# Kernel tuning notes

Hardware: AMD Instinct MI355X
Metric: run time of the kernel (lower is better)

Reference implementation:

```python
import jax, jax.numpy as jnp
import numpy as np

C = 256
C8 = C // 8
B, D, H, W = 1, 8, 32, 32
N = D * H * W


def setup_inputs() -> dict:
    key = jax.random.key(0)
    ks = jax.random.split(key, 16)
    s = 0.02
    inp = {
        'x': jax.random.normal(ks[0], (B, C, D, H, W), dtype=jnp.float32),
        'WqA': jax.random.normal(ks[1], (C8, C), dtype=jnp.float32) * s,
        'bqA': jnp.zeros((C8,), dtype=jnp.float32),
        'WkA': jax.random.normal(ks[2], (C8, C), dtype=jnp.float32) * s,
        'bkA': jnp.zeros((C8,), dtype=jnp.float32),
        'WvA': jax.random.normal(ks[3], (C, C), dtype=jnp.float32) * s,
        'bvA': jnp.zeros((C,), dtype=jnp.float32),
        'WqB': jax.random.normal(ks[4], (C8, C), dtype=jnp.float32) * s,
        'bqB': jnp.zeros((C8,), dtype=jnp.float32),
        'WkB': jax.random.normal(ks[5], (C8, C), dtype=jnp.float32) * s,
        'bkB': jnp.zeros((C8,), dtype=jnp.float32),
        'WvB': jax.random.normal(ks[6], (C, C), dtype=jnp.float32) * s,
        'bvB': jnp.zeros((C,), dtype=jnp.float32),
        'gamma_A': jax.random.normal(ks[7], (1,), dtype=jnp.float32) * 0.5,
        'gamma_B': jax.random.normal(ks[8], (1,), dtype=jnp.float32) * 0.5,
    }
    return inp


def _conv1x1(Wt, b, xf):
    # 1x1x1 Conv3d on flattened volume: [Cout,Cin] x [B,Cin,N] -> [B,Cout,N]
    return jnp.einsum('oc,bcn->bon', Wt, xf) + b[None, :, None]


def reference(x, WqA, bqA, WkA, bkA, WvA, bvA, WqB, bqB, WkB, bkB, WvB, bvB, gamma_A, gamma_B):
    b_, c_, d_, h_, w_ = x.shape
    n = d_ * h_ * w_
    xf = x.reshape(b_, c_, n)  # [B,C,N]

    QA = _conv1x1(WqA, bqA, xf)  # [B,C8,N]
    KA = _conv1x1(WkA, bkA, xf)
    VA = _conv1x1(WvA, bvA, xf)  # [B,C,N]
    QB = _conv1x1(WqB, bqB, xf)
    KB = _conv1x1(WkB, bkB, xf)
    VB = _conv1x1(WvB, bvB, xf)

    # attention_B_A[b,n,m] = softmax_m( QB^T KA )
    attn_BA = jax.nn.softmax(jnp.einsum('bcn,bcm->bnm', QB, KA), axis=-1)
    # F_B_new = V_A @ attn_BA^T
    F_B = jnp.einsum('bcm,bnm->bcn', VA, attn_BA).reshape(b_, c_, d_, h_, w_)

    attn_AB = jax.nn.softmax(jnp.einsum('bcn,bcm->bnm', QA, KB), axis=-1)
    F_A = jnp.einsum('bcm,bnm->bcn', VB, attn_AB).reshape(b_, c_, d_, h_, w_)

    out_task1 = gamma_A[0] * F_A + x
    out_task2 = gamma_B[0] * F_B + x
    return (out_task1, out_task2)
```

## Files before the change

kernel.cpp:

```cpp
#include <hip/hip_runtime.h>

#define N 8192
#define CIN 256
#define C8 32
#define QBLK 64
#define KVB 64
#define L2E 1.4426950408889634f

typedef __attribute__((ext_vector_type(8))) short short8;
typedef __attribute__((ext_vector_type(4))) float f32x4;
typedef __attribute__((ext_vector_type(4))) float float4_;
typedef __attribute__((ext_vector_type(4))) unsigned short ushort4_;
typedef __attribute__((ext_vector_type(2))) unsigned uint2_;

#define OFF_QTA 0u
#define OFF_KTA 262144u
#define OFF_QTB 524288u
#define OFF_KTB 786432u
#define OFF_VA  1048576u
#define OFF_VB  3145728u
#define PROJ_USHORTS 5242880u

__device__ __forceinline__ unsigned short f2bf(float f) {
    unsigned u = __builtin_bit_cast(unsigned, f);
    u += 0x7fffu + ((u >> 16) & 1u);
    return (unsigned short)(u >> 16);
}
__device__ __forceinline__ unsigned packbf2(float a, float b) {
    return (unsigned)f2bf(a) | ((unsigned)f2bf(b) << 16);
}
__device__ __forceinline__ float bf2f(unsigned short u) {
    return __builtin_bit_cast(float, (unsigned)u << 16);
}

__global__ __launch_bounds__(256) void castw_kernel(
    const float* __restrict__ WqA, const float* __restrict__ WkA, const float* __restrict__ WvA,
    const float* __restrict__ WqB, const float* __restrict__ WkB, const float* __restrict__ WvB,
    unsigned short* __restrict__ Wb)
{
    const int idx = blockIdx.x * 256 + threadIdx.x;
    const int e = idx * 4;
    const int r = e >> 8;
    const float* src; int rel;
    if (r < 32)       { src = WqA; rel = e; }
    else if (r < 64)  { src = WkA; rel = e - 32 * 256; }
    else if (r < 320) { src = WvA; rel = e - 64 * 256; }
    else if (r < 352) { src = WqB; rel = e - 320 * 256; }
    else if (r < 384) { src = WkB; rel = e - 352 * 256; }
    else              { src = WvB; rel = e - 384 * 256; }
    const float sc = (r < 32 || (r >= 320 && r < 352)) ? L2E : 1.0f;
    float4_ v = *(const float4_*)(src + rel);
    ushort4_ o;
    o.x = f2bf(v.x * sc); o.y = f2bf(v.y * sc); o.z = f2bf(v.z * sc); o.w = f2bf(v.w * sc);
    *(ushort4_*)(Wb + e) = o;
}

__global__ __launch_bounds__(512) void proj_kernel(
    const float* __restrict__ x, const unsigned short* __restrict__ Wb,
    const float* __restrict__ bqA, const float* __restrict__ bkA, const float* __restrict__ bvA,
    const float* __restrict__ bqB, const float* __restrict__ bkB, const float* __restrict__ bvB,
    unsigned short* __restrict__ ws)
{
    __shared__ __align__(16) unsigned short xT[32 * 256];

    const int tid = threadIdx.x;
    const int w = tid >> 6, l = tid & 63, g = l >> 4, lc = l & 15;
    const int n0 = blockIdx.x * 32;

    #pragma unroll
    for (int r = 0; r < 4; ++r) {
        const int flat4 = r * 512 + tid;
        const int c = flat4 >> 3, nl = (flat4 & 7) * 4;
        float4_ v = *(const float4_*)(x + (size_t)c * N + n0 + nl);
        #pragma unroll
        for (int e = 0; e < 4; ++e) {
            const int nn = nl + e;
            const int byte = nn * 512 + ((2 * c) ^ ((nn & 7) << 4));
            *(unsigned short*)((char*)xT + byte) = f2bf(v[e]);
        }
    }
    __syncthreads();

    f32x4 acc[5][2];
    #pragma unroll
    for (int i = 0; i < 5; ++i)
        #pragma unroll
        for (int ns = 0; ns < 2; ++ns) acc[i][ns] = (f32x4){0.f, 0.f, 0.f, 0.f};

    for (int c0 = 0; c0 < 256; c0 += 32) {
        short8 xf[2];
        #pragma unroll
        for (int ns = 0; ns < 2; ++ns) {
            const int byte = (ns * 16 + lc) * 512 + ((2 * (c0 + 8 * g)) ^ ((lc & 7) << 4));
            xf[ns] = *(const short8*)((const char*)xT + byte);
        }
        #pragma unroll
        for (int i = 0; i < 5; ++i) {
            const int ot = w * 5 + i;
            const short8 wf = *(const short8*)(Wb + (size_t)(ot * 16 + lc) * 256 + c0 + 8 * g);
            const bool isV = (ot >= 4 && ot < 20) || (ot >= 24);
            #pragma unroll
            for (int ns = 0; ns < 2; ++ns)
                acc[i][ns] = isV
                    ? __builtin_amdgcn_mfma_f32_16x16x32_bf16(wf, xf[ns], acc[i][ns], 0, 0, 0)
                    : __builtin_amdgcn_mfma_f32_16x16x32_bf16(xf[ns], wf, acc[i][ns], 0, 0, 0);
        }
    }

    #pragma unroll
    for (int i = 0; i < 5; ++i) {
        const int ot = w * 5 + i;
        const float* bias; unsigned short* dst; int orelm; bool isV = false; float bsc = 1.0f;
        if (ot < 2)       { bias = bqA; dst = ws + OFF_QTA; orelm = ot * 16;        bsc = L2E; }
        else if (ot < 4)  { bias = bkA; dst = ws + OFF_KTA; orelm = (ot - 2) * 16; }
        else if (ot < 20) { bias = bvA; dst = ws + OFF_VA;  orelm = (ot - 4) * 16;  isV = true; }
        else if (ot < 22) { bias = bqB; dst = ws + OFF_QTB; orelm = (ot - 20) * 16; bsc = L2E; }
        else if (ot < 24) { bias = bkB; dst = ws + OFF_KTB; orelm = (ot - 22) * 16; }
        else              { bias = bvB; dst = ws + OFF_VB;  orelm = (ot - 24) * 16; isV = true; }

        if (isV) {
            #pragma unroll
            for (int ii = 0; ii < 4; ++ii) {
                const float b = bias[orelm + 4 * g + ii];
                #pragma unroll
                for (int ns = 0; ns < 2; ++ns)
                    dst[(size_t)(orelm + 4 * g + ii) * N + n0 + ns * 16 + lc] = f2bf(acc[i][ns][ii] + b);
            }
        } else {
            const float b = bias[orelm + lc] * bsc;
            #pragma unroll
            for (int ns = 0; ns < 2; ++ns)
                #pragma unroll
                for (int ii = 0; ii < 4; ++ii)
                    dst[(size_t)(n0 + ns * 16 + 4 * g + ii) * C8 + orelm + lc] = f2bf(acc[i][ns][ii] + b);
        }
    }
}

__global__ __launch_bounds__(512, 4) void attn_kernel(
    const unsigned short* __restrict__ ws,
    unsigned short* __restrict__ accb,
    float* __restrict__ Lpart,
    int SP)
{
    __shared__ __align__(16) unsigned short Vt[2][256 * 64];
    __shared__ __align__(16) unsigned short Pl[2][64 * 64];

    const int tid = threadIdx.x;
    const int w = tid >> 6, l = tid & 63, g = l >> 4, lc = l & 15;
    const int bid = blockIdx.x;
    const int dir = bid & 1;
    const int qb  = (bid >> 1) & 127;
    const int sp  = bid >> 8;
    const int mlen   = N / SP;
    const int m_base = sp * mlen;
    const int NS     = mlen / KVB;

    const unsigned short* qt = ws + (dir ? OFF_QTA : OFF_QTB);
    const unsigned short* kt = ws + (dir ? OFF_KTB : OFF_KTA);
    const unsigned short* V  = ws + (dir ? OFF_VB  : OFF_VA);

    const bool sw = (w < 4);
    const int col = w * 16 + lc;

    short8 qf = {};
    if (sw) qf = *(const short8*)(qt + (size_t)(qb * QBLK + col) * C8 + 8 * g);

    const int src_c   = w * 32 + (l >> 3);
    const int src_swz = ((l & 7) ^ ((l >> 3) & 7)) << 3;
    #define STAGE(vb, mo)                                                                 \
        _Pragma("unroll")                                                                 \
        for (int h = 0; h < 4; ++h) {                                                     \
            const unsigned short* srcp = V + (size_t)(src_c + 8 * h) * N + (mo) + src_swz; \
            __builtin_amdgcn_global_load_lds(                                             \
                (const __attribute__((address_space(1))) unsigned*)srcp,                  \
                (__attribute__((address_space(3))) unsigned*)(&Vt[vb][(w * 32 + h * 8) * 64]), \
                16, 0, 0);                                                                \
        }

    STAGE(0, m_base)

    short8 kf[4], kfn[4];
    if (sw) {
        #pragma unroll
        for (int t = 0; t < 4; ++t)
            kf[t] = *(const short8*)(kt + (size_t)(m_base + 16 * t + lc) * C8 + 8 * g);
    }

    f32x4 acc[2][4];
    #pragma unroll
    for (int u = 0; u < 2; ++u)
        #pragma unroll
        for (int j = 0; j < 4; ++j) acc[u][j] = (f32x4){0.f, 0.f, 0.f, 0.f};
    float Lr = 0.f;

    for (int s = 0; s < NS; ++s) {
        const int m0 = m_base + s * KVB;
        const int pb = s & 1;

        if (sw) {
            if (s + 1 < NS) {
                #pragma unroll
                for (int t = 0; t < 4; ++t)
                    kfn[t] = *(const short8*)(kt + (size_t)(m0 + KVB + 16 * t + lc) * C8 + 8 * g);
            }
            f32x4 sv[4];
            #pragma unroll
            for (int t = 0; t < 4; ++t)
                sv[t] = __builtin_amdgcn_mfma_f32_16x16x32_bf16(kf[t], qf, (f32x4){0.f,0.f,0.f,0.f}, 0, 0, 0);

            float pr[4][4];
            #pragma unroll
            for (int t = 0; t < 4; ++t)
                #pragma unroll
                for (int i = 0; i < 4; ++i) {
                    pr[t][i] = __builtin_amdgcn_exp2f(sv[t][i]);
                    Lr += pr[t][i];
                }
            #pragma unroll
            for (int t = 0; t < 4; ++t) {
                uint2_ u2;
                u2.x = packbf2(pr[t][0], pr[t][1]);
                u2.y = packbf2(pr[t][2], pr[t][3]);
                const int byte = col * 128 + ((((2 * t + (g >> 1)) ^ (col & 7)) << 4)) + ((g & 1) << 3);
                *(uint2_*)((char*)Pl[pb] + byte) = u2;
            }
        }

        __syncthreads();

        if (s + 1 < NS) STAGE(pb ^ 1, m0 + KVB)

        __builtin_amdgcn_s_setprio(1);
        short8 vf[2][2];
        #pragma unroll
        for (int u = 0; u < 2; ++u)
            #pragma unroll
            for (int kc = 0; kc < 2; ++kc)
                vf[u][kc] = *(const short8*)((const char*)Vt[pb]
                              + (w * 32 + u * 16 + lc) * 128 + (((kc * 4 + g) ^ (lc & 7)) << 4));
        #pragma unroll
        for (int kc = 0; kc < 2; ++kc) {
            short8 pf[4];
            #pragma unroll
            for (int j = 0; j < 4; ++j)
                pf[j] = *(const short8*)((const char*)Pl[pb]
                          + (j * 16 + lc) * 128 + (((kc * 4 + g) ^ (lc & 7)) << 4));
            #pragma unroll
            for (int u = 0; u < 2; ++u)
                #pragma unroll
                for (int j = 0; j < 4; ++j)
                    acc[u][j] = __builtin_amdgcn_mfma_f32_16x16x32_bf16(vf[u][kc], pf[j], acc[u][j], 0, 0, 0);
        }
        __builtin_amdgcn_s_setprio(0);

        if (sw && s + 1 < NS) {
            #pragma unroll
            for (int t = 0; t < 4; ++t) kf[t] = kfn[t];
        }
    }

    if (sw) {
        Lr += __shfl_xor(Lr, 16);
        Lr += __shfl_xor(Lr, 32);
    }
    const size_t blk = (size_t)(dir * 128 + qb) * SP + sp;
    unsigned short* ab = accb + blk * (256 * 64);
    #pragma unroll
    for (int u = 0; u < 2; ++u)
        #pragma unroll
        for (int j = 0; j < 4; ++j)
            #pragma unroll
            for (int i = 0; i < 4; ++i) {
                const int c  = w * 32 + u * 16 + 4 * g + i;
                const int nl = j * 16 + lc;
                ab[c * 64 + nl] = f2bf(acc[u][j][i]);
            }
    if (sw && l < 16) Lpart[blk * 64 + w * 16 + l] = Lr;
}

__global__ __launch_bounds__(256) void combine_kernel(
    const float* __restrict__ x,
    const unsigned short* __restrict__ accb,
    const float* __restrict__ Lpart,
    const float* __restrict__ gammaA, const float* __restrict__ gammaB,
    float* __restrict__ out, int SP)
{
    const int tid = blockIdx.x * 256 + threadIdx.x;
    const int nl0 = (tid & 7) * 8;
    const int qb  = (tid >> 3) & 127;
    const int c   = (tid >> 10) & 255;
    const int dir = (tid >> 18) & 1;

    const size_t bb = (size_t)(dir * 128 + qb) * SP;
    float s[8], Ls[8];
    #pragma unroll
    for (int e = 0; e < 8; ++e) { s[e] = 0.f; Ls[e] = 0.f; }

    for (int sp = 0; sp < SP; ++sp) {
        const unsigned short* ap = accb + (bb + sp) * (256 * 64) + (size_t)c * 64 + nl0;
        const short8 av = *(const short8*)ap;
        const float* lp = Lpart + (bb + sp) * 64 + nl0;
        #pragma unroll
        for (int e = 0; e < 8; ++e) {
            s[e]  += bf2f((unsigned short)av[e]);
            Ls[e] += lp[e];
        }
    }

    const float gamma = dir ? gammaA[0] : gammaB[0];
    const size_t off = (size_t)c * N + qb * QBLK + nl0;
    const float* xp = x + off;
    float* op = out + (dir ? 0 : (size_t)CIN * N) + off;
    #pragma unroll
    for (int e = 0; e < 8; ++e) op[e] = gamma * s[e] / Ls[e] + xp[e];
}

extern "C" void kernel_launch(void* const* d_in, const int* in_sizes, int n_in,
                              void* d_out, int out_size, void* d_ws, size_t ws_size,
                              hipStream_t stream) {
    const float* x = (const float*)d_in[0];
    unsigned short* ws = (unsigned short*)d_ws;

    size_t needed4 = (size_t)PROJ_USHORTS * 2 + 4ull * 8388608 + 4ull * 65536;
    size_t needed2 = (size_t)PROJ_USHORTS * 2 + 2ull * 8388608 + 2ull * 65536;
    int SP = (ws_size >= needed4) ? 4 : (ws_size >= needed2) ? 2 : 1;

    unsigned short* accb = ws + PROJ_USHORTS;
    unsigned short* Wb   = accb;
    float* Lpart = (float*)(ws + PROJ_USHORTS + (size_t)SP * 4194304);

    castw_kernel<<<160, 256, 0, stream>>>(
        (const float*)d_in[1], (const float*)d_in[3], (const float*)d_in[5],
        (const float*)d_in[7], (const float*)d_in[9], (const float*)d_in[11], Wb);

    proj_kernel<<<256, 512, 0, stream>>>(
        x, Wb,
        (const float*)d_in[2],  (const float*)d_in[4],  (const float*)d_in[6],
        (const float*)d_in[8],  (const float*)d_in[10], (const float*)d_in[12],
        ws);

    attn_kernel<<<256 * SP, 512, 0, stream>>>(ws, accb, Lpart, SP);

    combine_kernel<<<2048, 256, 0, stream>>>(
        x, accb, Lpart,
        (const float*)d_in[13], (const float*)d_in[14],
        (float*)d_out, SP);
}
```

Baseline: 224.9 us.

## Restructure attention kernel: 128-query tiles, V in registers, drop LDS V staging

The attention kernel now handles 128 queries per block with all 8 waves computing scores, instead of 64 queries with half the waves idle during the score phase. V fragments are loaded from global memory straight into registers and double-buffered there, replacing the LDS staging through global_load_lds. The PV product is retiled so each wave owns a 64x64 output tile. The projection and combine kernels switch to vectorized packed stores to match the new layouts, and the split-K factor drops to at most 2, which halves the grid. The change raises register pressure and cuts block count, which risks lower occupancy and load balance.

New measurement: 319.4 us. 1.42x slower.

```diff
diff --git a/kernel.cpp b/kernel.cpp
--- a/kernel.cpp
+++ b/kernel.cpp
@@ -3,7 +3,7 @@
 #define N 8192
 #define CIN 256
 #define C8 32
-#define QBLK 64
+#define QBLK 128
 #define KVB 64
 #define L2E 1.4426950408889634f
 
@@ -102,8 +102,8 @@
             #pragma unroll
             for (int ns = 0; ns < 2; ++ns)
                 acc[i][ns] = isV
-                    ? __builtin_amdgcn_mfma_f32_16x16x32_bf16(wf, xf[ns], acc[i][ns], 0, 0, 0)
-                    : __builtin_amdgcn_mfma_f32_16x16x32_bf16(xf[ns], wf, acc[i][ns], 0, 0, 0);
+                    ? __builtin_amdgcn_mfma_f32_16x16x32_bf16(xf[ns], wf, acc[i][ns], 0, 0, 0)
+                    : __builtin_amdgcn_mfma_f32_16x16x32_bf16(wf, xf[ns], acc[i][ns], 0, 0, 0);
         }
     }
 
@@ -119,164 +119,149 @@
         else              { bias = bvB; dst = ws + OFF_VB;  orelm = (ot - 24) * 16; isV = true; }
 
         if (isV) {
-            #pragma unroll
-            for (int ii = 0; ii < 4; ++ii) {
-                const float b = bias[orelm + 4 * g + ii];
-                #pragma unroll
-                for (int ns = 0; ns < 2; ++ns)
-                    dst[(size_t)(orelm + 4 * g + ii) * N + n0 + ns * 16 + lc] = f2bf(acc[i][ns][ii] + b);
+            const float b = bias[orelm + lc];
+            #pragma unroll
+            for (int ns = 0; ns < 2; ++ns) {
+                ushort4_ pk;
+                pk.x = f2bf(acc[i][ns][0] + b); pk.y = f2bf(acc[i][ns][1] + b);
+                pk.z = f2bf(acc[i][ns][2] + b); pk.w = f2bf(acc[i][ns][3] + b);
+                *(ushort4_*)(dst + (size_t)(orelm + lc) * N + n0 + ns * 16 + 4 * g) = pk;
             }
         } else {
-            const float b = bias[orelm + lc] * bsc;
-            #pragma unroll
-            for (int ns = 0; ns < 2; ++ns)
+            #pragma unroll
+            for (int ns = 0; ns < 2; ++ns) {
+                ushort4_ pk;
                 #pragma unroll
                 for (int ii = 0; ii < 4; ++ii)
-                    dst[(size_t)(n0 + ns * 16 + 4 * g + ii) * C8 + orelm + lc] = f2bf(acc[i][ns][ii] + b);
-        }
-    }
-}
-
-__global__ __launch_bounds__(512, 4) void attn_kernel(
+                    pk[ii] = f2bf(acc[i][ns][ii] + bias[orelm + 4 * g + ii] * bsc);
+                *(ushort4_*)(dst + (size_t)(n0 + ns * 16 + lc) * C8 + orelm + 4 * g) = pk;
+            }
+        }
+    }
+}
+
+__global__ __launch_bounds__(512) void attn_kernel(
     const unsigned short* __restrict__ ws,
     unsigned short* __restrict__ accb,
     float* __restrict__ Lpart,
     int SP)
 {
-    __shared__ __align__(16) unsigned short Vt[2][256 * 64];
-    __shared__ __align__(16) unsigned short Pl[2][64 * 64];
+    __shared__ __align__(16) unsigned short Pl[2][QBLK * KVB];
 
     const int tid = threadIdx.x;
     const int w = tid >> 6, l = tid & 63, g = l >> 4, lc = l & 15;
     const int bid = blockIdx.x;
     const int dir = bid & 1;
-    const int qb  = (bid >> 1) & 127;
-    const int sp  = bid >> 8;
-    const int mlen   = N / SP;
-    const int m_base = sp * mlen;
-    const int NS     = mlen / KVB;
+    const int qb  = (bid >> 1) & 63;
+    const int sp  = bid >> 7;
+    const int mlen = N / SP, m_base = sp * mlen, NS = mlen / KVB;
 
     const unsigned short* qt = ws + (dir ? OFF_QTA : OFF_QTB);
     const unsigned short* kt = ws + (dir ? OFF_KTB : OFF_KTA);
     const unsigned short* V  = ws + (dir ? OFF_VB  : OFF_VA);
 
-    const bool sw = (w < 4);
-    const int col = w * 16 + lc;
-
-    short8 qf = {};
-    if (sw) qf = *(const short8*)(qt + (size_t)(qb * QBLK + col) * C8 + 8 * g);
-
-    const int src_c   = w * 32 + (l >> 3);
-    const int src_swz = ((l & 7) ^ ((l >> 3) & 7)) << 3;
-    #define STAGE(vb, mo)                                                                 \
-        _Pragma("unroll")                                                                 \
-        for (int h = 0; h < 4; ++h) {                                                     \
-            const unsigned short* srcp = V + (size_t)(src_c + 8 * h) * N + (mo) + src_swz; \
-            __builtin_amdgcn_global_load_lds(                                             \
-                (const __attribute__((address_space(1))) unsigned*)srcp,                  \
-                (__attribute__((address_space(3))) unsigned*)(&Vt[vb][(w * 32 + h * 8) * 64]), \
-                16, 0, 0);                                                                \
-        }
-
-    STAGE(0, m_base)
-
-    short8 kf[4], kfn[4];
-    if (sw) {
-        #pragma unroll
-        for (int t = 0; t < 4; ++t)
-            kf[t] = *(const short8*)(kt + (size_t)(m_base + 16 * t + lc) * C8 + 8 * g);
-    }
-
-    f32x4 acc[2][4];
-    #pragma unroll
-    for (int u = 0; u < 2; ++u)
-        #pragma unroll
-        for (int j = 0; j < 4; ++j) acc[u][j] = (f32x4){0.f, 0.f, 0.f, 0.f};
+    const int q0  = qb * QBLK;
+    const int myq = w * 16 + lc;
+    const int ct0 = (w >> 1) * 4;
+    const int cj0 = (w & 1) * 4;
+    const int sw7 = lc & 7;
+
+    const short8 qf = *(const short8*)(qt + (size_t)(q0 + myq) * C8 + 8 * g);
+
+    short8 kf[4], kfn[4], vf[4][2], vfn[4][2];
+    #pragma unroll
+    for (int t = 0; t < 4; ++t)
+        kf[t] = *(const short8*)(kt + (size_t)(m_base + 16 * t + lc) * C8 + 8 * g);
+    #pragma unroll
+    for (int u = 0; u < 4; ++u)
+        #pragma unroll
+        for (int kc = 0; kc < 2; ++kc)
+            vf[u][kc] = *(const short8*)(V + (size_t)((ct0 + u) * 16 + lc) * N + m_base + kc * 32 + 8 * g);
+
+    f32x4 acc[4][4];
+    #pragma unroll
+    for (int j = 0; j < 4; ++j)
+        #pragma unroll
+        for (int u = 0; u < 4; ++u) acc[j][u] = (f32x4){0.f, 0.f, 0.f, 0.f};
     float Lr = 0.f;
 
+    #pragma unroll 2
     for (int s = 0; s < NS; ++s) {
         const int m0 = m_base + s * KVB;
         const int pb = s & 1;
-
-        if (sw) {
-            if (s + 1 < NS) {
+        const bool more = (s + 1 < NS);
+
+        if (more) {
+            #pragma unroll
+            for (int t = 0; t < 4; ++t)
+                kfn[t] = *(const short8*)(kt + (size_t)(m0 + KVB + 16 * t + lc) * C8 + 8 * g);
+            #pragma unroll
+            for (int u = 0; u < 4; ++u)
                 #pragma unroll
-                for (int t = 0; t < 4; ++t)
-                    kfn[t] = *(const short8*)(kt + (size_t)(m0 + KVB + 16 * t + lc) * C8 + 8 * g);
+                for (int kc = 0; kc < 2; ++kc)
+                    vfn[u][kc] = *(const short8*)(V + (size_t)((ct0 + u) * 16 + lc) * N + m0 + KVB + kc * 32 + 8 * g);
+        }
+
+        f32x4 sv[4];
+        #pragma unroll
+        for (int t = 0; t < 4; ++t)
+            sv[t] = __builtin_amdgcn_mfma_f32_16x16x32_bf16(kf[t], qf, (f32x4){0.f,0.f,0.f,0.f}, 0, 0, 0);
+
+        #pragma unroll
+        for (int t = 0; t < 4; ++t) {
+            float p0 = __builtin_amdgcn_exp2f(sv[t][0]);
+            float p1 = __builtin_amdgcn_exp2f(sv[t][1]);
+            float p2 = __builtin_amdgcn_exp2f(sv[t][2]);
+            float p3 = __builtin_amdgcn_exp2f(sv[t][3]);
+            Lr += (p0 + p1) + (p2 + p3);
+            uint2_ u2; u2.x = packbf2(p0, p1); u2.y = packbf2(p2, p3);
+            const int byte = myq * 128 + (((2 * t + (g >> 1)) ^ sw7) << 4) + ((g & 1) << 3);
+            *(uint2_*)((char*)Pl[pb] + byte) = u2;
+        }
+
+        __syncthreads();
+
+        __builtin_amdgcn_s_setprio(1);
+        #pragma unroll
+        for (int j = 0; j < 4; ++j) {
+            const int q = (cj0 + j) * 16 + lc;
+            const short8 pf0 = *(const short8*)((const char*)Pl[pb] + q * 128 + ((g ^ sw7) << 4));
+            const short8 pf1 = *(const short8*)((const char*)Pl[pb] + q * 128 + (((4 + g) ^ sw7) << 4));
+            #pragma unroll
+            for (int u = 0; u < 4; ++u) {
+                acc[j][u] = __builtin_amdgcn_mfma_f32_16x16x32_bf16(pf0, vf[u][0], acc[j][u], 0, 0, 0);
+                acc[j][u] = __builtin_amdgcn_mfma_f32_16x16x32_bf16(pf1, vf[u][1], acc[j][u], 0, 0, 0);
             }
-            f32x4 sv[4];
-            #pragma unroll
-            for (int t = 0; t < 4; ++t)
-                sv[t] = __builtin_amdgcn_mfma_f32_16x16x32_bf16(kf[t], qf, (f32x4){0.f,0.f,0.f,0.f}, 0, 0, 0);
-
-            float pr[4][4];
-            #pragma unroll
-            for (int t = 0; t < 4; ++t)
+        }
+        __builtin_amdgcn_s_setprio(0);
+
+        if (more) {
+            #pragma unroll
+            for (int t = 0; t < 4; ++t) kf[t] = kfn[t];
+            #pragma unroll
+            for (int u = 0; u < 4; ++u)
                 #pragma unroll
-                for (int i = 0; i < 4; ++i) {
-                    pr[t][i] = __builtin_amdgcn_exp2f(sv[t][i]);
-                    Lr += pr[t][i];
-                }
-            #pragma unroll
-            for (int t = 0; t < 4; ++t) {
-                uint2_ u2;
-                u2.x = packbf2(pr[t][0], pr[t][1]);
-                u2.y = packbf2(pr[t][2], pr[t][3]);
-                const int byte = col * 128 + ((((2 * t + (g >> 1)) ^ (col & 7)) << 4)) + ((g & 1) << 3);
-                *(uint2_*)((char*)Pl[pb] + byte) = u2;
-            }
-        }
-
-        __syncthreads();
-
-        if (s + 1 < NS) STAGE(pb ^ 1, m0 + KVB)
-
-        __builtin_amdgcn_s_setprio(1);
-        short8 vf[2][2];
-        #pragma unroll
-        for (int u = 0; u < 2; ++u)
-            #pragma unroll
-            for (int kc = 0; kc < 2; ++kc)
-                vf[u][kc] = *(const short8*)((const char*)Vt[pb]
-                              + (w * 32 + u * 16 + lc) * 128 + (((kc * 4 + g) ^ (lc & 7)) << 4));
-        #pragma unroll
-        for (int kc = 0; kc < 2; ++kc) {
-            short8 pf[4];
-            #pragma unroll
-            for (int j = 0; j < 4; ++j)
-                pf[j] = *(const short8*)((const char*)Pl[pb]
-                          + (j * 16 + lc) * 128 + (((kc * 4 + g) ^ (lc & 7)) << 4));
-            #pragma unroll
-            for (int u = 0; u < 2; ++u)
-                #pragma unroll
-                for (int j = 0; j < 4; ++j)
-                    acc[u][j] = __builtin_amdgcn_mfma_f32_16x16x32_bf16(vf[u][kc], pf[j], acc[u][j], 0, 0, 0);
-        }
-        __builtin_amdgcn_s_setprio(0);
-
-        if (sw && s + 1 < NS) {
-            #pragma unroll
-            for (int t = 0; t < 4; ++t) kf[t] = kfn[t];
-        }
-    }
-
-    if (sw) {
-        Lr += __shfl_xor(Lr, 16);
-        Lr += __shfl_xor(Lr, 32);
-    }
-    const size_t blk = (size_t)(dir * 128 + qb) * SP + sp;
-    unsigned short* ab = accb + blk * (256 * 64);
-    #pragma unroll
-    for (int u = 0; u < 2; ++u)
-        #pragma unroll
-        for (int j = 0; j < 4; ++j)
-            #pragma unroll
-            for (int i = 0; i < 4; ++i) {
-                const int c  = w * 32 + u * 16 + 4 * g + i;
-                const int nl = j * 16 + lc;
-                ab[c * 64 + nl] = f2bf(acc[u][j][i]);
-            }
-    if (sw && l < 16) Lpart[blk * 64 + w * 16 + l] = Lr;
+                for (int kc = 0; kc < 2; ++kc) vf[u][kc] = vfn[u][kc];
+        }
+    }
+
+    Lr += __shfl_xor(Lr, 16);
+    Lr += __shfl_xor(Lr, 32);
+
+    const size_t blk = (size_t)(dir * 64 + qb) * SP + sp;
+    unsigned short* ab = accb + blk * (size_t)(CIN * QBLK);
+    #pragma unroll
+    for (int j = 0; j < 4; ++j)
+        #pragma unroll
+        for (int u = 0; u < 4; ++u) {
+            const int c = (ct0 + u) * 16 + lc;
+            const int qloc = (cj0 + j) * 16 + 4 * g;
+            ushort4_ pk;
+            pk.x = f2bf(acc[j][u][0]); pk.y = f2bf(acc[j][u][1]);
+            pk.z = f2bf(acc[j][u][2]); pk.w = f2bf(acc[j][u][3]);
+            *(ushort4_*)(ab + (size_t)c * QBLK + qloc) = pk;
+        }
+    if (l < 16) Lpart[blk * QBLK + w * 16 + l] = Lr;
 }
 
 __global__ __launch_bounds__(256) void combine_kernel(
@@ -287,20 +272,20 @@
     float* __restrict__ out, int SP)
 {
     const int tid = blockIdx.x * 256 + threadIdx.x;
-    const int nl0 = (tid & 7) * 8;
-    const int qb  = (tid >> 3) & 127;
+    const int nl0 = (tid & 15) * 8;
+    const int qb  = (tid >> 4) & 63;
     const int c   = (tid >> 10) & 255;
     const int dir = (tid >> 18) & 1;
 
-    const size_t bb = (size_t)(dir * 128 + qb) * SP;
+    const size_t bb = (size_t)(dir * 64 + qb) * SP;
     float s[8], Ls[8];
     #pragma unroll
     for (int e = 0; e < 8; ++e) { s[e] = 0.f; Ls[e] = 0.f; }
 
     for (int sp = 0; sp < SP; ++sp) {
-        const unsigned short* ap = accb + (bb + sp) * (256 * 64) + (size_t)c * 64 + nl0;
+        const unsigned short* ap = accb + (bb + sp) * (size_t)(CIN * QBLK) + (size_t)c * QBLK + nl0;
         const short8 av = *(const short8*)ap;
-        const float* lp = Lpart + (bb + sp) * 64 + nl0;
+        const float* lp = Lpart + (bb + sp) * QBLK + nl0;
         #pragma unroll
         for (int e = 0; e < 8; ++e) {
             s[e]  += bf2f((unsigned short)av[e]);
@@ -322,13 +307,14 @@
     const float* x = (const float*)d_in[0];
     unsigned short* ws = (unsigned short*)d_ws;
 
-    size_t needed4 = (size_t)PROJ_USHORTS * 2 + 4ull * 8388608 + 4ull * 65536;
-    size_t needed2 = (size_t)PROJ_USHORTS * 2 + 2ull * 8388608 + 2ull * 65536;
-    int SP = (ws_size >= needed4) ? 4 : (ws_size >= needed2) ? 2 : 1;
+    const size_t accb_us_per_sp = 128ull * CIN * QBLK;
+    const size_t lpart_f_per_sp = 128ull * QBLK;
+    size_t needed2 = (size_t)PROJ_USHORTS * 2 + 2 * accb_us_per_sp * 2 + 2 * lpart_f_per_sp * 4;
+    int SP = (ws_size >= needed2) ? 2 : 1;
 
     unsigned short* accb = ws + PROJ_USHORTS;
     unsigned short* Wb   = accb;
-    float* Lpart = (float*)(ws + PROJ_USHORTS + (size_t)SP * 4194304);
+    float* Lpart = (float*)(ws + PROJ_USHORTS + (size_t)SP * accb_us_per_sp);
 
     castw_kernel<<<160, 256, 0, stream>>>(
         (const float*)d_in[1], (const float*)d_in[3], (const float*)d_in[5],
@@ -340,7 +326,7 @@
         (const float*)d_in[8],  (const float*)d_in[10], (const float*)d_in[12],
         ws);
 
-    attn_kernel<<<256 * SP, 512, 0, stream>>>(ws, accb, Lpart, SP);
+    attn_kernel<<<128 * SP, 512, 0, stream>>>(ws, accb, Lpart, SP);
 
     combine_kernel<<<2048, 256, 0, stream>>>(
         x, accb, Lpart,
```
